# Optimization experiments

Hardware: AMD Instinct MI355X
Metric: run time of the kernel (lower is better)

## Reference

```python
import jax, jax.numpy as jnp
import numpy as np
from jax import lax

WINDOW_SIZE = 11
SIGMA = 1.5
VAL_RANGE = 1000.0 / 10.0  # L = 100.0


def _gaussian_window(window_size, sigma, channel):
    # matches torch: exp(-(x - ws//2)^2 / (2*sigma^2)), normalized
    x = np.arange(window_size, dtype=np.float32)
    g = np.exp(-((x - window_size // 2) ** 2) / (2.0 * sigma ** 2))
    g = g / g.sum()
    w2d = np.outer(g, g).astype(np.float32)  # [ws, ws]
    # depthwise kernel, OIHW with I=1, O=channel
    w = np.broadcast_to(w2d, (channel, 1, window_size, window_size))
    return jnp.asarray(np.ascontiguousarray(w))


def _depthwise_conv(x, window, channel):
    # x: [B, C, H, W], window: [C, 1, ws, ws], valid padding, groups=C
    return lax.conv_general_dilated(
        x, window,
        window_strides=(1, 1), padding='VALID',
        dimension_numbers=('NCHW', 'OIHW', 'NCHW'),
        feature_group_count=channel)


def setup_inputs() -> dict:
    key = jax.random.key(0)
    k1, k2 = jax.random.split(key)
    B, C, H, W = 32, 1, 480, 640
    img1 = jax.random.uniform(k1, (B, C, H, W), dtype=jnp.float32)
    img2 = jax.random.uniform(k2, (B, C, H, W), dtype=jnp.float32)
    return {"img1": img1, "img2": img2}


def reference(img1, img2):
    channel = img1.shape[1]
    window = _gaussian_window(WINDOW_SIZE, SIGMA, channel)

    L = VAL_RANGE
    C1 = (0.01 * L) ** 2
    C2 = (0.03 * L) ** 2

    mu1 = _depthwise_conv(img1, window, channel)
    mu2 = _depthwise_conv(img2, window, channel)
    mu1_sq = mu1 * mu1
    mu2_sq = mu2 * mu2
    mu1_mu2 = mu1 * mu2

    sigma1_sq = _depthwise_conv(img1 * img1, window, channel) - mu1_sq
    sigma2_sq = _depthwise_conv(img2 * img2, window, channel) - mu2_sq
    sigma12 = _depthwise_conv(img1 * img2, window, channel) - mu1_mu2

    v1 = 2.0 * sigma12 + C2
    v2 = sigma1_sq + sigma2_sq + C2
    ssim_map = (2.0 * mu1_mu2 + C1) * v1 / ((mu1_sq + mu2_sq + C1) * v2)

    ret = jnp.mean(ssim_map)  # size_average=True
    L_ssim = (1.0 - ret) / 2.0
    return L_ssim
```

## Files before the change

kernel.cpp:

```cpp
#include <hip/hip_runtime.h>

#define IMG_H 480
#define IMG_W 640
#define OUT_H 470
#define OUT_W 630
#define NBATCH 32
#define SW 118
#define NSTRIPE 6
#define RCH 47
#define NCHUNK 10
#define NROWS (RCH + 10)

#define SSIM_C1 1.0f
#define SSIM_C2 9.0f

typedef float v2f __attribute__((ext_vector_type(2)));

__device__ constexpr float WG[11] = {
    0.00102838f, 0.00759876f, 0.03600077f, 0.10936068f, 0.21300554f,
    0.26601173f,
    0.21300554f, 0.10936068f, 0.03600077f, 0.00759876f, 0.00102838f
};

__device__ __forceinline__ float lane_shift(int baddr, int j, float v) {
    return __int_as_float(
        __builtin_amdgcn_ds_bpermute(baddr + (j << 2), __float_as_int(v)));
}

__device__ __forceinline__ v2f pk_fma(v2f a, v2f b, v2f c) {
    return __builtin_elementwise_fma(a, b, c);
}

#define STEP(IT, PP)                                                          \
  {                                                                           \
    const int P   = (PP) % 11;                                                \
    const int cur = (PP) & 1;                                                 \
    const int nxt = ((PP) + 1) & 1;                                           \
          \
    int gy = y0 + (IT) + 2; if (gy > IMG_H - 1) gy = IMG_H - 1;               \
    const float2 n1 = *(const float2*)(p1 + gy * IMG_W + colA);               \
    const float2 n2 = *(const float2*)(p2 + gy * IMG_W + colA);               \
         \
                                  \
    pv[nxt][0] = (v2f){c1.x, c2.x};                                           \
    pv[nxt][1] = (v2f){c1.y, c2.y};                                           \
    _Pragma("unroll")                                                         \
    for (int j = 1; j <= 5; ++j) {                                            \
      pv[nxt][2*j]   = (v2f){lane_shift(baddr, j, c1.x),                      \
                             lane_shift(baddr, j, c2.x)};                     \
      pv[nxt][2*j+1] = (v2f){lane_shift(baddr, j, c1.y),                      \
                             lane_shift(baddr, j, c2.y)};                     \
    }                                                                         \
               \
    v2f ph[2], phs[2]; float ph12[2];                                         \
    ph[0] = (v2f){0.f,0.f}; ph[1] = (v2f){0.f,0.f};                           \
    phs[0] = (v2f){0.f,0.f}; phs[1] = (v2f){0.f,0.f};                         \
    ph12[0] = 0.f; ph12[1] = 0.f;                                             \
    _Pragma("unroll")                                                         \
    for (int j = 0; j < 11; ++j) {                                            \
      const v2f wj = (v2f){WG[j], WG[j]};                                     \
      _Pragma("unroll")                                                       \
      for (int s = 0; s < 2; ++s) {                                           \
        const v2f v = pv[cur][j + s];                                         \
        const v2f t = wj * v;                       \
        ph[s] += t;                                 \
        phs[s] = pk_fma(t, v, phs[s]);              \
        ph12[s] = fmaf(t.x, v.y, ph12[s]);          \
      }                                                                       \
    }                                                                         \
           \
    _Pragma("unroll")                                                         \
    for (int sl = 0; sl < 11; ++sl) {                                         \
      const float wt = WG[(P - sl + 11) % 11];                                \
      const v2f wv = (v2f){wt, wt};                                           \
      _Pragma("unroll")                                                       \
      for (int s = 0; s < 2; ++s) {                                           \
        acc_mu[sl][s] = pk_fma(wv, ph[s],  acc_mu[sl][s]);                    \
        acc_sq[sl][s] = pk_fma(wv, phs[s], acc_sq[sl][s]);                    \
        acc_x[sl][s]  = fmaf(wt, ph12[s],  acc_x[sl][s]);                     \
      }                                                                       \
    }                                                                         \
         \
    const int sc = (P + 1) % 11;                                              \
    if ((IT) >= 10 && (y0 + (IT) - 10) < OUT_H) {                             \
      _Pragma("unroll")                                                       \
      for (int s = 0; s < 2; ++s) {                                           \
        if (s == 0 ? validA : validB) {                                       \
          const v2f m = acc_mu[sc][s];                        \
          const v2f msq = m * m;                          \
          const float mu12 = m.x * m.y;                                       \
          const v2f sg = acc_sq[sc][s] - msq;                 \
          const float vA = fmaf(2.f, acc_x[sc][s] - mu12, SSIM_C2);           \
          const float vB = sg.x + sg.y + SSIM_C2;                             \
          const float num = fmaf(2.f, mu12, SSIM_C1) * vA;                    \
          const float den = (msq.x + msq.y + SSIM_C1) * vB;                   \
          lsum = fmaf(num, __builtin_amdgcn_rcpf(den), lsum);                 \
        }                                                                     \
      }                                                                       \
    }                                                                         \
    _Pragma("unroll")                                                         \
    for (int s = 0; s < 2; ++s) {                                             \
      acc_mu[sc][s] = (v2f){0.f,0.f};                                         \
      acc_sq[sc][s] = (v2f){0.f,0.f};                                         \
      acc_x[sc][s]  = 0.f;                                                    \
    }                                                                         \
                                        \
    c1 = n1; c2 = n2;                                                         \
  }

__global__ __launch_bounds__(64, 2) void ssim_main(
    const float* __restrict__ img1,
    const float* __restrict__ img2,
    float* __restrict__ partials)
{
    const int lane   = threadIdx.x;
    const int stripe = blockIdx.x;
    const int cy     = blockIdx.y;
    const int b      = blockIdx.z;
    const int x0 = SW * stripe;
    const int y0 = RCH * cy;

    const float* __restrict__ p1 = img1 + (size_t)b * (IMG_H * IMG_W);
    const float* __restrict__ p2 = img2 + (size_t)b * (IMG_H * IMG_W);

    int colA = x0 + 2 * lane;  if (colA > IMG_W - 2) colA = IMG_W - 2;
    const int baddr = lane << 2;

    const bool validA = (lane < 59) && (x0 + 2 * lane     < OUT_W);
    const bool validB = (lane < 59) && (x0 + 2 * lane + 1 < OUT_W);

    v2f acc_mu[11][2], acc_sq[11][2];
    float acc_x[11][2];
#pragma unroll
    for (int i = 0; i < 11; ++i)
#pragma unroll
        for (int s = 0; s < 2; ++s) {
            acc_mu[i][s] = (v2f){0.f, 0.f};
            acc_sq[i][s] = (v2f){0.f, 0.f};
            acc_x[i][s] = 0.f;
        }

    float lsum = 0.f;

    v2f pv[2][12];

    float2 c1, c2;
    {
        const float2 r1 = *(const float2*)(p1 + y0 * IMG_W + colA);
        const float2 r2 = *(const float2*)(p2 + y0 * IMG_W + colA);
        pv[0][0] = (v2f){r1.x, r2.x};
        pv[0][1] = (v2f){r1.y, r2.y};
#pragma unroll
        for (int j = 1; j <= 5; ++j) {
            pv[0][2*j]   = (v2f){lane_shift(baddr, j, r1.x),
                                 lane_shift(baddr, j, r2.x)};
            pv[0][2*j+1] = (v2f){lane_shift(baddr, j, r1.y),
                                 lane_shift(baddr, j, r2.y)};
        }
        c1 = *(const float2*)(p1 + (y0 + 1) * IMG_W + colA);
        c2 = *(const float2*)(p2 + (y0 + 1) * IMG_W + colA);
    }

    for (int blk = 0; blk < 2; ++blk) {
        const int base = 22 * blk;
#pragma unroll
        for (int p = 0; p < 22; ++p) STEP(base + p, p)
    }
#pragma unroll
    for (int p = 0; p < 13; ++p) STEP(44 + p, p)

#pragma unroll
    for (int off = 32; off > 0; off >>= 1)
        lsum += __shfl_down(lsum, off);
    if (lane == 0)
        partials[(b * NCHUNK + cy) * NSTRIPE + stripe] = lsum;
}

__global__ __launch_bounds__(256) void ssim_reduce(
    const float* __restrict__ partials, float* __restrict__ out)
{
    const int n = NSTRIPE * NCHUNK * NBATCH;
    __shared__ double red[256];
    int tid = threadIdx.x;
    double s = 0.0;
    for (int i = tid; i < n; i += 256) s += (double)partials[i];
    red[tid] = s;
    __syncthreads();
    for (int k = 128; k > 0; k >>= 1) {
        if (tid < k) red[tid] += red[tid + k];
        __syncthreads();
    }
    if (tid == 0) {
        double mean = red[0] / (double)((size_t)NBATCH * OUT_H * OUT_W);
        out[0] = (float)((1.0 - mean) * 0.5);
    }
}

extern "C" void kernel_launch(void* const* d_in, const int* in_sizes, int n_in,
                              void* d_out, int out_size, void* d_ws, size_t ws_size,
                              hipStream_t stream)
{
    const float* img1 = (const float*)d_in[0];
    const float* img2 = (const float*)d_in[1];
    float* out = (float*)d_out;
    float* partials = (float*)d_ws;

    dim3 grid(NSTRIPE, NCHUNK, NBATCH);
    ssim_main<<<grid, dim3(64), 0, stream>>>(img1, img2, partials);
    ssim_reduce<<<1, dim3(256), 0, stream>>>(partials, out);
}
```

Before: 134.3 us.

## Replace cross-lane bpermute row sharing with direct 12-float loads per lane

```diff
diff --git a/kernel.cpp b/kernel.cpp
--- a/kernel.cpp
+++ b/kernel.cpp
@@ -22,11 +22,6 @@
     0.21300554f, 0.10936068f, 0.03600077f, 0.00759876f, 0.00102838f
 };
 
-__device__ __forceinline__ float lane_shift(int baddr, int j, float v) {
-    return __int_as_float(
-        __builtin_amdgcn_ds_bpermute(baddr + (j << 2), __float_as_int(v)));
-}
-
 __device__ __forceinline__ v2f pk_fma(v2f a, v2f b, v2f c) {
     return __builtin_elementwise_fma(a, b, c);
 }
@@ -36,76 +31,66 @@
     const int P   = (PP) % 11;                                                \
     const int cur = (PP) & 1;                                                 \
     const int nxt = ((PP) + 1) & 1;                                           \
-          \
-    int gy = y0 + (IT) + 2; if (gy > IMG_H - 1) gy = IMG_H - 1;               \
-    const float2 n1 = *(const float2*)(p1 + gy * IMG_W + colA);               \
-    const float2 n2 = *(const float2*)(p2 + gy * IMG_W + colA);               \
-         \
-                                  \
-    pv[nxt][0] = (v2f){c1.x, c2.x};                                           \
-    pv[nxt][1] = (v2f){c1.y, c2.y};                                           \
-    _Pragma("unroll")                                                         \
-    for (int j = 1; j <= 5; ++j) {                                            \
-      pv[nxt][2*j]   = (v2f){lane_shift(baddr, j, c1.x),                      \
-                             lane_shift(baddr, j, c2.x)};                     \
-      pv[nxt][2*j+1] = (v2f){lane_shift(baddr, j, c1.y),                      \
-                             lane_shift(baddr, j, c2.y)};                     \
+     \
+    {                                                                         \
+      int gy = y0 + (IT) + 1; if (gy > IMG_H - 1) gy = IMG_H - 1;             \
+      const float* __restrict__ r1 = p1 + gy * IMG_W + colA;                  \
+      const float* __restrict__ r2 = p2 + gy * IMG_W + colA;                  \
+      _Pragma("unroll")                                                       \
+      for (int k = 0; k < 6; ++k) {                                           \
+        pb[nxt][0][k] = *(const v2f*)(r1 + 2 * k);                            \
+        pb[nxt][1][k] = *(const v2f*)(r2 + 2 * k);                            \
+      }                                                                       \
     }                                                                         \
-               \
-    v2f ph[2], phs[2]; float ph12[2];                                         \
-    ph[0] = (v2f){0.f,0.f}; ph[1] = (v2f){0.f,0.f};                           \
-    phs[0] = (v2f){0.f,0.f}; phs[1] = (v2f){0.f,0.f};                         \
-    ph12[0] = 0.f; ph12[1] = 0.f;                                             \
+            \
+    v2f h1  = (v2f){0.f,0.f}, h2  = (v2f){0.f,0.f};                           \
+    v2f h11 = (v2f){0.f,0.f}, h22 = (v2f){0.f,0.f}, h12 = (v2f){0.f,0.f};     \
     _Pragma("unroll")                                                         \
     for (int j = 0; j < 11; ++j) {                                            \
       const v2f wj = (v2f){WG[j], WG[j]};                                     \
-      _Pragma("unroll")                                                       \
-      for (int s = 0; s < 2; ++s) {                                           \
-        const v2f v = pv[cur][j + s];                                         \
-        const v2f t = wj * v;                       \
-        ph[s] += t;                                 \
-        phs[s] = pk_fma(t, v, phs[s]);              \
-        ph12[s] = fmaf(t.x, v.y, ph12[s]);          \
+      v2f q1, q2;                                                             \
+      if (j & 1) {                                                            \
+        q1 = (v2f){pb[cur][0][j >> 1].y, pb[cur][0][(j >> 1) + 1].x};         \
+        q2 = (v2f){pb[cur][1][j >> 1].y, pb[cur][1][(j >> 1) + 1].x};         \
+      } else {                                                                \
+        q1 = pb[cur][0][j >> 1];                                              \
+        q2 = pb[cur][1][j >> 1];                                              \
       }                                                                       \
+      const v2f t1 = wj * q1;                                                 \
+      const v2f t2 = wj * q2;                                                 \
+      h1 += t1; h2 += t2;                                                     \
+      h11 = pk_fma(t1, q1, h11);                                              \
+      h22 = pk_fma(t2, q2, h22);                                              \
+      h12 = pk_fma(t1, q2, h12);                                              \
     }                                                                         \
-           \
+                              \
     _Pragma("unroll")                                                         \
     for (int sl = 0; sl < 11; ++sl) {                                         \
       const float wt = WG[(P - sl + 11) % 11];                                \
       const v2f wv = (v2f){wt, wt};                                           \
-      _Pragma("unroll")                                                       \
-      for (int s = 0; s < 2; ++s) {                                           \
-        acc_mu[sl][s] = pk_fma(wv, ph[s],  acc_mu[sl][s]);                    \
-        acc_sq[sl][s] = pk_fma(wv, phs[s], acc_sq[sl][s]);                    \
-        acc_x[sl][s]  = fmaf(wt, ph12[s],  acc_x[sl][s]);                     \
-      }                                                                       \
+      acc[sl][0] = pk_fma(wv, h1,  acc[sl][0]);                               \
+      acc[sl][1] = pk_fma(wv, h2,  acc[sl][1]);                               \
+      acc[sl][2] = pk_fma(wv, h11, acc[sl][2]);                               \
+      acc[sl][3] = pk_fma(wv, h22, acc[sl][3]);                               \
+      acc[sl][4] = pk_fma(wv, h12, acc[sl][4]);                               \
     }                                                                         \
-         \
+          \
     const int sc = (P + 1) % 11;                                              \
     if ((IT) >= 10 && (y0 + (IT) - 10) < OUT_H) {                             \
-      _Pragma("unroll")                                                       \
-      for (int s = 0; s < 2; ++s) {                                           \
-        if (s == 0 ? validA : validB) {                                       \
-          const v2f m = acc_mu[sc][s];                        \
-          const v2f msq = m * m;                          \
-          const float mu12 = m.x * m.y;                                       \
-          const v2f sg = acc_sq[sc][s] - msq;                 \
-          const float vA = fmaf(2.f, acc_x[sc][s] - mu12, SSIM_C2);           \
-          const float vB = sg.x + sg.y + SSIM_C2;                             \
-          const float num = fmaf(2.f, mu12, SSIM_C1) * vA;                    \
-          const float den = (msq.x + msq.y + SSIM_C1) * vB;                   \
-          lsum = fmaf(num, __builtin_amdgcn_rcpf(den), lsum);                 \
-        }                                                                     \
-      }                                                                       \
+      const v2f m1 = acc[sc][0], m2 = acc[sc][1];                             \
+      const v2f msq1 = m1 * m1, msq2 = m2 * m2, mu12 = m1 * m2;               \
+      const v2f two = (v2f){2.f, 2.f};                                        \
+      const v2f c1v = (v2f){SSIM_C1, SSIM_C1};                                \
+      const v2f c2v = (v2f){SSIM_C2, SSIM_C2};                                \
+      const v2f vA = pk_fma(two, acc[sc][4] - mu12, c2v);                     \
+      const v2f vB = (acc[sc][2] - msq1) + (acc[sc][3] - msq2) + c2v;         \
+      const v2f num = pk_fma(two, mu12, c1v) * vA;                            \
+      const v2f den = (msq1 + msq2 + c1v) * vB;                               \
+      if (validA) lsum = fmaf(num.x, __builtin_amdgcn_rcpf(den.x), lsum);     \
+      if (validB) lsum = fmaf(num.y, __builtin_amdgcn_rcpf(den.y), lsum);     \
     }                                                                         \
     _Pragma("unroll")                                                         \
-    for (int s = 0; s < 2; ++s) {                                             \
-      acc_mu[sc][s] = (v2f){0.f,0.f};                                         \
-      acc_sq[sc][s] = (v2f){0.f,0.f};                                         \
-      acc_x[sc][s]  = 0.f;                                                    \
-    }                                                                         \
-                                        \
-    c1 = n1; c2 = n2;                                                         \
+    for (int ch = 0; ch < 5; ++ch) acc[sc][ch] = (v2f){0.f, 0.f};             \
   }
 
 __global__ __launch_bounds__(64, 2) void ssim_main(
@@ -123,42 +108,30 @@
     const float* __restrict__ p1 = img1 + (size_t)b * (IMG_H * IMG_W);
     const float* __restrict__ p2 = img2 + (size_t)b * (IMG_H * IMG_W);
 
-    int colA = x0 + 2 * lane;  if (colA > IMG_W - 2) colA = IMG_W - 2;
-    const int baddr = lane << 2;
+    int colA = x0 + 2 * lane;
+    if (colA > IMG_W - 12) colA = IMG_W - 12;
 
     const bool validA = (lane < 59) && (x0 + 2 * lane     < OUT_W);
     const bool validB = (lane < 59) && (x0 + 2 * lane + 1 < OUT_W);
 
-    v2f acc_mu[11][2], acc_sq[11][2];
-    float acc_x[11][2];
+    v2f acc[11][5];
 #pragma unroll
     for (int i = 0; i < 11; ++i)
 #pragma unroll
-        for (int s = 0; s < 2; ++s) {
-            acc_mu[i][s] = (v2f){0.f, 0.f};
-            acc_sq[i][s] = (v2f){0.f, 0.f};
-            acc_x[i][s] = 0.f;
-        }
+        for (int ch = 0; ch < 5; ++ch) acc[i][ch] = (v2f){0.f, 0.f};
 
     float lsum = 0.f;
 
-    v2f pv[2][12];
+    v2f pb[2][2][6];
 
-    float2 c1, c2;
     {
-        const float2 r1 = *(const float2*)(p1 + y0 * IMG_W + colA);
-        const float2 r2 = *(const float2*)(p2 + y0 * IMG_W + colA);
-        pv[0][0] = (v2f){r1.x, r2.x};
-        pv[0][1] = (v2f){r1.y, r2.y};
+        const float* __restrict__ r1 = p1 + y0 * IMG_W + colA;
+        const float* __restrict__ r2 = p2 + y0 * IMG_W + colA;
 #pragma unroll
-        for (int j = 1; j <= 5; ++j) {
-            pv[0][2*j]   = (v2f){lane_shift(baddr, j, r1.x),
-                                 lane_shift(baddr, j, r2.x)};
-            pv[0][2*j+1] = (v2f){lane_shift(baddr, j, r1.y),
-                                 lane_shift(baddr, j, r2.y)};
+        for (int k = 0; k < 6; ++k) {
+            pb[0][0][k] = *(const v2f*)(r1 + 2 * k);
+            pb[0][1][k] = *(const v2f*)(r2 + 2 * k);
         }
-        c1 = *(const float2*)(p1 + (y0 + 1) * IMG_W + colA);
-        c2 = *(const float2*)(p2 + (y0 + 1) * IMG_W + colA);
     }
 
     for (int blk = 0; blk < 2; ++blk) {
```

New measurement: 129.6 us. 1.04x faster.
